# Kernel tuning notes

Hardware: AMD Instinct MI355X
Metric: run time of the kernel (lower is better)

Reference implementation:

```python
import jax, jax.numpy as jnp
import numpy as np

DECAY = 0.99
EPS = 1e-05


def setup_inputs() -> dict:
    key = jax.random.key(0)
    k1, k2 = jax.random.split(key)
    B, L, D, K = 8, 2048, 512, 4096
    x = jax.random.normal(k1, (B, L, D), dtype=jnp.float32)
    # variance_scaling(scale=1, fan_in, uniform): U(-limit, limit), limit = sqrt(3/fan_in)
    limit = np.sqrt(3.0 / D)
    codebook = jax.random.uniform(k2, (K, D), dtype=jnp.float32, minval=-limit, maxval=limit)
    return {
        "x": x,
        "codebook": codebook,
        "hidden_cluster": jnp.zeros((K,), jnp.float32),
        "hidden_dw": jnp.zeros((K, D), jnp.float32),
        "count": jnp.zeros((), jnp.float32),
    }


def reference(x, codebook, hidden_cluster, hidden_dw, count):
    K, D = codebook.shape
    B, L, _ = x.shape
    # avoids materializing the (B,L,K,D) broadcast the naive cdist creates)
    x2 = jnp.sum(x * x, axis=-1, keepdims=True)                  # (B,L,1)
    c2 = jnp.sum(codebook * codebook, axis=-1)                   # (K,)
    xc = jnp.einsum("bld,kd->blk", x, codebook)                  # (B,L,K)
    d2 = x2 - 2.0 * xc + c2
    indices = jnp.argmin(d2, axis=-1)                            # (B,L) int
    flat_idx = indices.reshape(-1)

    # cluster_counts = one_hot(indices).sum((0,1)) as a scatter-add
    cluster_counts = jnp.zeros((K,), jnp.float32).at[flat_idx].add(1.0)
    # dw = einsum('bln,bld->nd', one_hot, x) as a scatter-add of x rows
    dw = jnp.zeros((K, D), jnp.float32).at[flat_idx].add(x.reshape(-1, D))

    decay = jnp.asarray(DECAY, x.dtype)
    one = jnp.ones([], x.dtype)
    count_new = count + 1.0
    bias = one - decay ** count_new

    hidden_cluster_new = hidden_cluster * decay + (one - decay) * cluster_counts
    avg_cluster = hidden_cluster_new / bias
    hidden_dw_new = hidden_dw * decay + (one - decay) * dw
    avg_dw = hidden_dw_new / bias

    N = jnp.sum(avg_cluster)
    cc = (avg_cluster + EPS) / (N + K * EPS) * N
    codebook_new = avg_dw / cc[:, None]

    # quantized = one_hot(indices) @ codebook_new == gather
    q = codebook_new[indices]                                    # (B,L,D)
    quantized = x + jax.lax.stop_gradient(q - x)
    # optax.l2_loss(x, quantized).mean() == 0.5*(x-quantized)^2 mean
    codebook_loss = 0.5 * jnp.mean(jnp.square(x - quantized))
    return quantized, codebook_loss, indices
```

## Files before the change

### kernel.cpp

```cpp
#include <hip/hip_runtime.h>
#include <math.h>

#define BL 16384
#define D  512
#define K  4096
#define NCHB 8
#define XLOFF 8388608

#define OFF_C2    0
#define OFF_X2    (16<<10)
#define OFF_CNT   (80<<10)
#define OFF_AVGC  (96<<10)
#define OFF_SCAL  (112<<10)
#define OFF_IDX16 (116<<10)
#define OFF_KEYS  (160<<10)
#define OFF_CAND  (288<<10)
#define OFF_CBP   (576<<10)
#define OFF_CBN_FB (256<<10)

typedef _Float16 f16x8 __attribute__((ext_vector_type(8)));
typedef float    f32x4 __attribute__((ext_vector_type(4)));
#define MFMA16(a,b,c) __builtin_amdgcn_mfma_f32_16x16x32_f16(a,b,c,0,0,0)


__global__ void rowsq_all(const float* __restrict__ x, const float* __restrict__ cb,
                          float* __restrict__ x2, float* __restrict__ c2)
{
    int b    = blockIdx.x;
    int lane = threadIdx.x;
    const float* p; float* o; int row;
    if (b < K) { p = cb; o = c2; row = b; }
    else       { p = x;  o = x2; row = b - K; }
    p += (size_t)row * D;
    float s = 0.f;
#pragma unroll
    for (int j = 0; j < D / 64; ++j) {
        float v = p[lane + j * 64];
        s = fmaf(v, v, s);
    }
#pragma unroll
    for (int off = 32; off > 0; off >>= 1)
        s += __shfl_down(s, off, 64);
    if (lane == 0) o[row] = s;
}

__global__ __launch_bounds__(256) void rescore_kernel(
    const float* __restrict__ x, const float* __restrict__ cb,
    const float* __restrict__ x2, const float* __restrict__ c2,
    const unsigned short* __restrict__ cand,
    unsigned long long* __restrict__ keys,
    float* __restrict__ counts, unsigned short* __restrict__ idx16)
{
    int t = blockIdx.x * 256 + threadIdx.x;
    int row = t >> 3, ci = t & 7;
    int idx = cand[(size_t)row * 8 + ci];
    const float* xp = x  + (size_t)row * D;
    const float* cp = cb + (size_t)idx * D;
    float acc = 0.f;
#pragma unroll 4
    for (int k0 = 0; k0 < D; k0 += 4) {
        float4 xv = *(const float4*)(xp + k0);
        float4 cv = *(const float4*)(cp + k0);
        acc = fmaf(xv.x, cv.x, acc);
        acc = fmaf(xv.y, cv.y, acc);
        acc = fmaf(xv.z, cv.z, acc);
        acc = fmaf(xv.w, cv.w, acc);
    }
    float wv = x2[row] - 2.0f * acc;
    float dd = wv + c2[idx];
    unsigned long long key =
        ((unsigned long long)__float_as_uint(dd) << 12) | (unsigned long long)idx;
#pragma unroll
    for (int m = 1; m < 8; m <<= 1) {
        unsigned long long o = __shfl_xor(key, m, 64);
        key = o < key ? o : key;
    }
    if ((t & 7) == 0) {
        keys[row] = key;
        int kf = (int)(key & 0xFFFULL);
        idx16[row] = (unsigned short)kf;
        atomicAdd(&counts[kf], 1.0f);
    }
}


__device__ __forceinline__ void load_lds16(const unsigned short* g, unsigned short* l) {
    __builtin_amdgcn_global_load_lds(
        (const __attribute__((address_space(1))) unsigned int*)(g),
        (__attribute__((address_space(3))) unsigned int*)(l), 16, 0, 0);
}

__global__ __launch_bounds__(256) void split_interleave(
    const float* __restrict__ x, const float* __restrict__ cb,
    unsigned short* __restrict__ xp, unsigned short* __restrict__ cbp)
{
    int gw   = blockIdx.x * 4 + (threadIdx.x >> 6);
    int lane = threadIdx.x & 63;
    int rl   = lane >> 3;
    int p    = lane & 7;
    const float* src; int nr, c, r0; bool isX;
    if (gw < 16384) { c = gw >> 11; r0 = (gw & 2047) * 8; src = x;  nr = BL; isX = true; }
    else { int lw = gw - 16384; c = lw >> 9; r0 = (lw & 511) * 8; src = cb; nr = K; isX = false; }
    int r = r0 + rl;
    int g = p ^ rl;
    const float* sp = src + (size_t)r * D + c * 64 + g * 8;
    float4 f0 = *(const float4*)sp, f1 = *(const float4*)(sp + 4);
    float f[8] = {f0.x,f0.y,f0.z,f0.w,f1.x,f1.y,f1.z,f1.w};
    __align__(16) _Float16 oh[8], ol[8];
#pragma unroll
    for (int i = 0; i < 8; ++i) {
        _Float16 h = (_Float16)f[i];
        oh[i] = h;
        ol[i] = (_Float16)(f[i] - (float)h);
    }
    size_t off = ((size_t)(c * nr + r) * 8 + p) * 8;
    if (isX) {
        *(uint4*)(xp + off)         = *(const uint4*)oh;
        *(uint4*)(xp + XLOFF + off) = *(const uint4*)ol;
    } else {
        *(uint4*)(cbp + off) = *(const uint4*)oh;
    }
}

__global__ __launch_bounds__(256, 2) void argmin_mfma(
    const unsigned short* __restrict__ xp, const unsigned short* __restrict__ cbp,
    const float* __restrict__ x2, const float* __restrict__ c2,
    unsigned short* __restrict__ cand)
{
    __shared__ __align__(16) unsigned short sAh[128 * 64];
    __shared__ __align__(16) unsigned short sAl[128 * 64];
    __shared__ __align__(16) unsigned short sB [128 * 64];

    const int tid = threadIdx.x;
    const int l   = tid & 63;
    const int w   = tid >> 6;
    const int wm  = w >> 1, wn = w & 1;
    const int q   = l >> 4;
    const int cc  = l & 15;
    const int row0 = blockIdx.x * 128;
    const int nb   = blockIdx.y * 1024;

    int rdA[4], rdB[4];
#pragma unroll
    for (int t = 0; t < 4; ++t) {
        int ra = wm * 64 + t * 16 + cc;
        int rb = wn * 64 + t * 16 + cc;
        rdA[t] = ra * 128 + ((q ^ (ra & 7)) * 16);
        rdB[t] = rb * 128 + ((q ^ (rb & 7)) * 16);
    }

    unsigned long long k1[16], k2[16];
#pragma unroll
    for (int s = 0; s < 16; ++s) { k1[s] = ~0ULL; k2[s] = ~0ULL; }

    for (int n0 = 0; n0 < 8; ++n0) {
        f32x4 acc[4][4];
#pragma unroll
        for (int tm = 0; tm < 4; ++tm)
#pragma unroll
            for (int tn = 0; tn < 4; ++tn) { f32x4 z = {0.f,0.f,0.f,0.f}; acc[tm][tn] = z; }

        for (int c = 0; c < NCHB; ++c) {
            __syncthreads();
            {
                size_t abase = ((size_t)c * BL + row0) * 64;
                size_t bbase = ((size_t)c * K + nb + n0 * 128) * 64;
#pragma unroll
                for (int i = 0; i < 12; ++i) {
                    int gi = i * 4 + w;
                    if (gi < 16)
                        load_lds16(xp + abase + gi * 512 + l * 8, &sAh[gi * 512 + l * 8]);
                    else if (gi < 32) {
                        int ga = gi - 16;
                        load_lds16(xp + XLOFF + abase + ga * 512 + l * 8, &sAl[ga * 512 + l * 8]);
                    } else {
                        int gb = gi - 32;
                        load_lds16(cbp + bbase + gb * 512 + l * 8, &sB[gb * 512 + l * 8]);
                    }
                }
            }
            __syncthreads();
#pragma unroll
            for (int kh = 0; kh < 2; ++kh) {
                const int xo = kh * 64;
                f16x8 Ah[4], Al[4], Bf[4];
#pragma unroll
                for (int t = 0; t < 4; ++t) {
                    Ah[t] = *(const f16x8*)((const char*)sAh + (rdA[t] ^ xo));
                    Al[t] = *(const f16x8*)((const char*)sAl + (rdA[t] ^ xo));
                    Bf[t] = *(const f16x8*)((const char*)sB  + (rdB[t] ^ xo));
                }
#pragma unroll
                for (int tm = 0; tm < 4; ++tm)
#pragma unroll
                    for (int tn = 0; tn < 4; ++tn) {
                        acc[tm][tn] = MFMA16(Ah[tm], Bf[tn], acc[tm][tn]);
                        acc[tm][tn] = MFMA16(Al[tm], Bf[tn], acc[tm][tn]);
                    }
            }
        }
        float c2v[4];
#pragma unroll
        for (int tn = 0; tn < 4; ++tn)
            c2v[tn] = c2[nb + n0 * 128 + wn * 64 + tn * 16 + cc];
#pragma unroll
        for (int tm = 0; tm < 4; ++tm)
#pragma unroll
            for (int r = 0; r < 4; ++r) {
                int s = tm * 4 + r;
                float x2v = x2[row0 + wm * 64 + tm * 16 + q * 4 + r];
#pragma unroll
                for (int tn = 0; tn < 4; ++tn) {
                    unsigned col = nb + n0 * 128 + wn * 64 + tn * 16 + cc;
                    float dd = (x2v - 2.0f * acc[tm][tn][r]) + c2v[tn];
                    unsigned long long key =
                        ((unsigned long long)__float_as_uint(dd) << 12) | col;
                    if (key < k1[s]) { k2[s] = k1[s]; k1[s] = key; }
                    else if (key < k2[s]) { k2[s] = key; }
                }
            }
    }

#pragma unroll
    for (int s = 0; s < 16; ++s) {
#pragma unroll
        for (int m = 1; m < 16; m <<= 1) {
            unsigned long long o1 = __shfl_xor(k1[s], m, 64);
            unsigned long long o2 = __shfl_xor(k2[s], m, 64);
            unsigned long long lf = k1[s] > o1 ? k1[s] : o1;
            unsigned long long ws_ = k2[s] < o2 ? k2[s] : o2;
            k1[s] = k1[s] < o1 ? k1[s] : o1;
            k2[s] = lf < ws_ ? lf : ws_;
        }
    }

    __syncthreads();
    unsigned long long* sc = (unsigned long long*)sAh;
    if (cc == 0) {
#pragma unroll
        for (int s = 0; s < 16; ++s) {
            int rl = wm * 64 + (s >> 2) * 16 + q * 4 + (s & 3);
            sc[(rl * 2 + wn) * 2 + 0] = k1[s];
            sc[(rl * 2 + wn) * 2 + 1] = k2[s];
        }
    }
    __syncthreads();
    if (tid < 128) {
        unsigned long long pa1 = sc[(tid * 2 + 0) * 2 + 0], pa2 = sc[(tid * 2 + 0) * 2 + 1];
        unsigned long long pb1 = sc[(tid * 2 + 1) * 2 + 0], pb2 = sc[(tid * 2 + 1) * 2 + 1];
        unsigned long long m1 = pa1 < pb1 ? pa1 : pb1;
        unsigned long long lf = pa1 > pb1 ? pa1 : pb1;
        unsigned long long ws_ = pa2 < pb2 ? pa2 : pb2;
        unsigned long long m2 = lf < ws_ ? lf : ws_;
        size_t base = (size_t)(row0 + tid) * 8 + blockIdx.y * 2;
        cand[base + 0] = (unsigned short)(m1 & 0xFFFULL);
        cand[base + 1] = (unsigned short)(m2 & 0xFFFULL);
    }
}

__global__ __launch_bounds__(256) void argmin_fb(
    const float* __restrict__ x, const float* __restrict__ cb,
    const float* __restrict__ x2, const float* __restrict__ c2,
    unsigned long long* __restrict__ keys)
{
    __shared__ __align__(16) float As[32][68];
    __shared__ __align__(16) float Bs[32][68];
    __shared__ float rv[64][16];
    __shared__ int   ri[64][16];

    const int tid  = threadIdx.x;
    const int tx   = tid & 15;
    const int ty   = tid >> 4;
    const int row0 = blockIdx.x * 64;
    const int nb   = blockIdx.y * 1024;

    float x2r[4];
#pragma unroll
    for (int m = 0; m < 4; ++m) x2r[m] = x2[row0 + ty * 4 + m];

    float minv[4]; int mini[4];
#pragma unroll
    for (int m = 0; m < 4; ++m) { minv[m] = 3.4028235e38f; mini[m] = 0; }

    for (int n0 = 0; n0 < 1024; n0 += 64) {
        float acc[4][4];
#pragma unroll
        for (int m = 0; m < 4; ++m)
#pragma unroll
            for (int n = 0; n < 4; ++n) acc[m][n] = 0.f;

        for (int d0 = 0; d0 < D; d0 += 32) {
            __syncthreads();
#pragma unroll
            for (int j = 0; j < 2; ++j) {
                int v   = j * 256 + tid;
                int row = v >> 3;
                int col = (v & 7) * 4;
                float4 av = *(const float4*)(x  + (size_t)(row0 + row) * D + d0 + col);
                As[col + 0][row] = av.x; As[col + 1][row] = av.y;
                As[col + 2][row] = av.z; As[col + 3][row] = av.w;
                float4 bv = *(const float4*)(cb + (size_t)(nb + n0 + row) * D + d0 + col);
                Bs[col + 0][row] = bv.x; Bs[col + 1][row] = bv.y;
                Bs[col + 2][row] = bv.z; Bs[col + 3][row] = bv.w;
            }
            __syncthreads();
#pragma unroll
            for (int kk = 0; kk < 32; ++kk) {
                float4 a4 = *(const float4*)&As[kk][ty * 4];
                float4 b4 = *(const float4*)&Bs[kk][tx * 4];
                float a_[4] = { a4.x, a4.y, a4.z, a4.w };
                float b_[4] = { b4.x, b4.y, b4.z, b4.w };
#pragma unroll
                for (int m = 0; m < 4; ++m)
#pragma unroll
                    for (int n = 0; n < 4; ++n)
                        acc[m][n] = fmaf(a_[m], b_[n], acc[m][n]);
            }
        }
#pragma unroll
        for (int n = 0; n < 4; ++n) {
            int kidx = nb + n0 + tx * 4 + n;
            float c2k = c2[kidx];
#pragma unroll
            for (int m = 0; m < 4; ++m) {
                float wv = x2r[m] - 2.0f * acc[m][n];
                float dd = wv + c2k;
                if (dd < minv[m]) { minv[m] = dd; mini[m] = kidx; }
            }
        }
    }
#pragma unroll
    for (int m = 0; m < 4; ++m) { rv[ty * 4 + m][tx] = minv[m]; ri[ty * 4 + m][tx] = mini[m]; }
    __syncthreads();
    if (tid < 64) {
        float bv = rv[tid][0]; int bi = ri[tid][0];
#pragma unroll
        for (int j = 1; j < 16; ++j) {
            float v = rv[tid][j]; int ii = ri[tid][j];
            if (v < bv || (v == bv && ii < bi)) { bv = v; bi = ii; }
        }
        unsigned long long key =
            ((unsigned long long)__float_as_uint(bv) << 12) | (unsigned long long)bi;
        atomicMin(&keys[row0 + tid], key);
    }
}


__global__ void count_kernel(const unsigned long long* __restrict__ keys,
                             float* __restrict__ counts, unsigned short* __restrict__ idx16)
{
    int i = blockIdx.x * 256 + threadIdx.x;
    int k = (int)(keys[i] & 0xFFFULL);
    idx16[i] = (unsigned short)k;
    atomicAdd(&counts[k], 1.0f);
}

__global__ __launch_bounds__(256) void ema_cluster_kernel(
    const float* __restrict__ hc, const float* __restrict__ counts,
    const float* __restrict__ countp, float* __restrict__ avgc, float* __restrict__ Nout)
{
    __shared__ float sm[256];
    int i = blockIdx.x * 256 + threadIdx.x;
    const float om = 1.0f - 0.99f;
    float bias = 1.0f - powf(0.99f, countp[0] + 1.0f);
    float a = (hc[i] * 0.99f + om * counts[i]) / bias;
    avgc[i] = a;
    sm[threadIdx.x] = a;
    __syncthreads();
    for (int s = 128; s > 0; s >>= 1) {
        if (threadIdx.x < s) sm[threadIdx.x] += sm[threadIdx.x + s];
        __syncthreads();
    }
    if (threadIdx.x == 0) atomicAdd(Nout, sm[0]);
}

__global__ __launch_bounds__(256) void code_update_kernel(
    const float* __restrict__ x, const unsigned short* __restrict__ idx16,
    const float* __restrict__ hdw, const float* __restrict__ avgc,
    const float* __restrict__ Nptr, const float* __restrict__ countp,
    float* __restrict__ cbn)
{
    __shared__ unsigned short rows[2048];
    __shared__ int cnt;
    int k = blockIdx.x, tid = threadIdx.x;
    if (tid == 0) cnt = 0;
    __syncthreads();
    const uint4* ip = (const uint4*)idx16;
    for (int j = 0; j < 8; ++j) {
        int u = j * 256 + tid;
        uint4 v = ip[u];
        unsigned ww[4] = {v.x, v.y, v.z, v.w};
#pragma unroll
        for (int e = 0; e < 4; ++e) {
            int k0 = (int)(ww[e] & 0xFFFFu), k1 = (int)(ww[e] >> 16);
            if (k0 == k) { int p = atomicAdd(&cnt, 1); if (p < 2048) rows[p] = (unsigned short)(u * 8 + e * 2); }
            if (k1 == k) { int p = atomicAdd(&cnt, 1); if (p < 2048) rows[p] = (unsigned short)(u * 8 + e * 2 + 1); }
        }
    }
    __syncthreads();
    int n = cnt < 2048 ? cnt : 2048;
    float a0 = 0.f, a1 = 0.f;
    for (int p = 0; p < n; ++p) {
        int r = rows[p];
        a0 += x[(size_t)r * D + tid];
        a1 += x[(size_t)r * D + tid + 256];
    }
    const float om = 1.0f - 0.99f;
    float bias = 1.0f - powf(0.99f, countp[0] + 1.0f);
    float Nv = *Nptr;
    float ccv = ((avgc[k] + 1e-5f) / (Nv + 0.04096f)) * Nv;
    size_t b = (size_t)k * D;
    cbn[b + tid]       = ((hdw[b + tid]       * 0.99f + om * a0) / bias) / ccv;
    cbn[b + tid + 256] = ((hdw[b + tid + 256] * 0.99f + om * a1) / bias) / ccv;
}

__global__ __launch_bounds__(256) void gather_kernel(
    const float* __restrict__ x, const unsigned long long* __restrict__ keys,
    const float* __restrict__ cbn, float* __restrict__ outq,
    float* __restrict__ partial)
{
    __shared__ float sm[256];
    int row = blockIdx.x;
    int tid = threadIdx.x;
    int k   = (int)(keys[row] & 0xFFFULL);
    const float* xpp = x   + (size_t)row * D;
    const float* cp  = cbn + (size_t)k   * D;
    float* op = outq + (size_t)row * D;
    float local = 0.f;
#pragma unroll
    for (int j = 0; j < 2; ++j) {
        int d = tid + j * 256;
        float xv = xpp[d];
        float qv = cp[d];
        float quant = xv + (qv - xv);
        op[d] = quant;
        float diff = xv - quant;
        local = fmaf(diff, diff, local);
    }
    sm[tid] = local;
    __syncthreads();
    for (int s = 128; s > 0; s >>= 1) {
        if (tid < s) sm[tid] += sm[tid + s];
        __syncthreads();
    }
    if (tid == 0) {
        partial[row] = sm[0];
        outq[8388609 + row] = (float)k;
    }
}

__global__ __launch_bounds__(256) void finalize_kernel(
    const float* __restrict__ partial, float* __restrict__ out)
{
    __shared__ double sm[256];
    int tid = threadIdx.x;
    double s = 0.0;
#pragma unroll
    for (int j = 0; j < 64; ++j) s += (double)partial[tid + j * 256];
    sm[tid] = s;
    __syncthreads();
    for (int st = 128; st > 0; st >>= 1) {
        if (tid < st) sm[tid] += sm[tid + st];
        __syncthreads();
    }
    if (tid == 0) out[8388608] = (float)(0.5 * sm[0] / 8388608.0);
}


extern "C" void kernel_launch(void* const* d_in, const int* in_sizes, int n_in,
                              void* d_out, int out_size, void* d_ws, size_t ws_size,
                              hipStream_t stream)
{
    const float* x   = (const float*)d_in[0];
    const float* cb  = (const float*)d_in[1];
    const float* hc  = (const float*)d_in[2];
    const float* hdw = (const float*)d_in[3];
    const float* cnt = (const float*)d_in[4];
    float* out = (float*)d_out;

    char* ws = (char*)d_ws;
    float*  c2     = (float*)(ws + OFF_C2);
    float*  x2     = (float*)(ws + OFF_X2);
    float*  counts = (float*)(ws + OFF_CNT);
    float*  avgc   = (float*)(ws + OFF_AVGC);
    float*  Nout   = (float*)(ws + OFF_SCAL + 8);
    unsigned short* idx16 = (unsigned short*)(ws + OFF_IDX16);
    unsigned long long* keys = (unsigned long long*)(ws + OFF_KEYS);
    float*  partial= (float*)(ws + OFF_X2);

    hipMemsetAsync(ws + OFF_CNT, 0, (32 << 10) + 16, stream);

    rowsq_all<<<K + BL, 64, 0, stream>>>(x, cb, x2, c2);

    const bool primary = ws_size >= ((size_t)10 << 20);
    float* cbn;
    if (primary) {
        unsigned short* gxp = (unsigned short*)d_out;
        unsigned short* gcp = (unsigned short*)(ws + OFF_CBP);
        unsigned short* cand = (unsigned short*)(ws + OFF_CAND);
        cbn = (float*)(ws + OFF_CBP);

        split_interleave<<<5120, 256, 0, stream>>>(x, cb, gxp, gcp);
        argmin_mfma<<<dim3(BL / 128, 4), 256, 0, stream>>>(gxp, gcp, x2, c2, cand);
        rescore_kernel<<<(BL * 8) / 256, 256, 0, stream>>>(x, cb, x2, c2, cand, keys,
                                                           counts, idx16);
    } else {
        cbn = (float*)(ws + OFF_CBN_FB);
        hipMemsetAsync(ws + OFF_KEYS, 0xFF, BL * 8, stream);
        argmin_fb<<<dim3(BL / 64, 4), 256, 0, stream>>>(x, cb, x2, c2, keys);
        count_kernel<<<BL / 256, 256, 0, stream>>>(keys, counts, idx16);
    }

    ema_cluster_kernel<<<K / 256, 256, 0, stream>>>(hc, counts, cnt, avgc, Nout);
    code_update_kernel<<<K, 256, 0, stream>>>(x, idx16, hdw, avgc, Nout, cnt, cbn);
    gather_kernel<<<BL, 256, 0, stream>>>(x, keys, cbn, out, partial);
    finalize_kernel<<<1, 256, 0, stream>>>(partial, out);
}
```

Baseline: 332.8 us.

## Double-buffer argmin MFMA loads with 8-wave blocks and interleaved compute phases

Rewrites the argmin GEMM main loop to use 512-thread blocks (2x4 waves), a 256-column N tile and double-buffered LDS. Global-to-LDS copies for the next k-chunk are issued in four slices, each overlapping one MFMA phase, with explicit waitcnt, barriers and raised wave priority around the MFMAs. c2 and x2 are staged in LDS once per block, and the final reduction now merges four wave partials. The aim is to hide memory latency behind MFMA work and drop the two full block syncs per chunk. In exchange it uses more LDS (128 KB buffers) and more barriers, and the hand-written wait counts add a risk of ordering errors.

Measured after the change: 349.5 us. +5.0%, slower.

```diff
diff --git a/kernel.cpp b/kernel.cpp
--- a/kernel.cpp
+++ b/kernel.cpp
@@ -122,23 +122,30 @@
     }
 }
 
-__global__ __launch_bounds__(256, 2) void argmin_mfma(
+__global__ __launch_bounds__(512, 2) void argmin_mfma(
     const unsigned short* __restrict__ xp, const unsigned short* __restrict__ cbp,
     const float* __restrict__ x2, const float* __restrict__ c2,
     unsigned short* __restrict__ cand)
 {
-    __shared__ __align__(16) unsigned short sAh[128 * 64];
-    __shared__ __align__(16) unsigned short sAl[128 * 64];
-    __shared__ __align__(16) unsigned short sB [128 * 64];
+    __shared__ __align__(16) unsigned short buf[2 * 32768];
+    __shared__ __align__(16) float c2s[1024];
+    __shared__ __align__(16) float x2s[128];
+
+#define AH_OFF 0
+#define AL_OFF 16384
+#define B_OFF  32768
 
     const int tid = threadIdx.x;
     const int l   = tid & 63;
-    const int w   = tid >> 6;
-    const int wm  = w >> 1, wn = w & 1;
     const int q   = l >> 4;
     const int cc  = l & 15;
+    const int w   = tid >> 6;
+    const int wm  = w >> 2;
+    const int wn  = w & 3;
     const int row0 = blockIdx.x * 128;
     const int nb   = blockIdx.y * 1024;
+
+    char* sb = (char*)buf;
 
     int rdA[4], rdB[4];
 #pragma unroll
@@ -149,76 +156,173 @@
         rdB[t] = rb * 128 + ((q ^ (rb & 7)) * 16);
     }
 
+    if (tid < 128) x2s[tid] = x2[row0 + tid];
+#pragma unroll
+    for (int j = 0; j < 2; ++j) c2s[tid + j * 512] = c2[nb + tid + j * 512];
+    {
+        const unsigned short* sAh0 = xp + ((size_t)row0 << 6);
+        const unsigned short* sAl0 = sAh0 + XLOFF;
+        const unsigned short* sB0  = cbp + ((size_t)nb << 6);
+#pragma unroll
+        for (int i = 0; i < 2; ++i) {
+            load_lds16(sAh0 + i * 4096 + tid * 8,
+                       (unsigned short*)(sb + AH_OFF + i * 8192 + tid * 16));
+            load_lds16(sAl0 + i * 4096 + tid * 8,
+                       (unsigned short*)(sb + AL_OFF + i * 8192 + tid * 16));
+        }
+#pragma unroll
+        for (int i = 0; i < 4; ++i)
+            load_lds16(sB0 + i * 4096 + tid * 8,
+                       (unsigned short*)(sb + B_OFF + i * 8192 + tid * 16));
+    }
+    asm volatile("s_waitcnt vmcnt(0) lgkmcnt(0)" ::: "memory");
+    __builtin_amdgcn_s_barrier();
+
     unsigned long long k1[16], k2[16];
 #pragma unroll
     for (int s = 0; s < 16; ++s) { k1[s] = ~0ULL; k2[s] = ~0ULL; }
 
-    for (int n0 = 0; n0 < 8; ++n0) {
-        f32x4 acc[4][4];
+    f32x4 acc[4][4];
+#pragma unroll
+    for (int tm = 0; tm < 4; ++tm)
+#pragma unroll
+        for (int tn = 0; tn < 4; ++tn) { f32x4 z = {0.f,0.f,0.f,0.f}; acc[tm][tn] = z; }
+
+#pragma unroll 1
+    for (int it = 0; it < 32; ++it) {
+        const bool pf = (it < 31);
+        const int  br = (it & 1) << 16;
+        const int  bw = br ^ 65536;
+        const int  it1 = it + 1;
+        const int  c1  = it1 & 7;
+        const int  n01 = (it1 >> 3) & 3;
+        const unsigned short* srcAh = xp + ((size_t)(c1 * BL + row0) << 6);
+        const unsigned short* srcAl = srcAh + XLOFF;
+        const unsigned short* srcB  = cbp + ((size_t)(c1 * K + nb + n01 * 256) << 6);
+
+        f16x8 Ah[4], Bf[4];
+#pragma unroll
+        for (int t = 0; t < 4; ++t) {
+            Ah[t] = *(const f16x8*)(sb + br + AH_OFF + rdA[t]);
+            Bf[t] = *(const f16x8*)(sb + br + B_OFF  + rdB[t]);
+        }
+        if (pf) {
+#pragma unroll
+            for (int i = 0; i < 2; ++i)
+                load_lds16(srcAh + i * 4096 + tid * 8,
+                           (unsigned short*)(sb + bw + AH_OFF + i * 8192 + tid * 16));
+            asm volatile("s_waitcnt vmcnt(2)" ::: "memory");
+        } else {
+            asm volatile("s_waitcnt vmcnt(0)" ::: "memory");
+        }
+        __builtin_amdgcn_s_barrier();
+        asm volatile("s_waitcnt lgkmcnt(0)" ::: "memory");
+        __builtin_amdgcn_sched_barrier(0);
+        __builtin_amdgcn_s_setprio(1);
 #pragma unroll
         for (int tm = 0; tm < 4; ++tm)
 #pragma unroll
-            for (int tn = 0; tn < 4; ++tn) { f32x4 z = {0.f,0.f,0.f,0.f}; acc[tm][tn] = z; }
-
-        for (int c = 0; c < NCHB; ++c) {
-            __syncthreads();
-            {
-                size_t abase = ((size_t)c * BL + row0) * 64;
-                size_t bbase = ((size_t)c * K + nb + n0 * 128) * 64;
-#pragma unroll
-                for (int i = 0; i < 12; ++i) {
-                    int gi = i * 4 + w;
-                    if (gi < 16)
-                        load_lds16(xp + abase + gi * 512 + l * 8, &sAh[gi * 512 + l * 8]);
-                    else if (gi < 32) {
-                        int ga = gi - 16;
-                        load_lds16(xp + XLOFF + abase + ga * 512 + l * 8, &sAl[ga * 512 + l * 8]);
-                    } else {
-                        int gb = gi - 32;
-                        load_lds16(cbp + bbase + gb * 512 + l * 8, &sB[gb * 512 + l * 8]);
+            for (int tn = 0; tn < 4; ++tn)
+                acc[tm][tn] = MFMA16(Ah[tm], Bf[tn], acc[tm][tn]);
+        __builtin_amdgcn_s_setprio(0);
+        __builtin_amdgcn_s_barrier();
+
+        f16x8 Al[4];
+#pragma unroll
+        for (int t = 0; t < 4; ++t)
+            Al[t] = *(const f16x8*)(sb + br + AL_OFF + rdA[t]);
+        if (pf) {
+#pragma unroll
+            for (int i = 0; i < 2; ++i)
+                load_lds16(srcB + i * 4096 + tid * 8,
+                           (unsigned short*)(sb + bw + B_OFF + i * 8192 + tid * 16));
+        }
+        __builtin_amdgcn_s_barrier();
+        asm volatile("s_waitcnt lgkmcnt(0)" ::: "memory");
+        __builtin_amdgcn_sched_barrier(0);
+        __builtin_amdgcn_s_setprio(1);
+#pragma unroll
+        for (int tm = 0; tm < 4; ++tm)
+#pragma unroll
+            for (int tn = 0; tn < 4; ++tn)
+                acc[tm][tn] = MFMA16(Al[tm], Bf[tn], acc[tm][tn]);
+        __builtin_amdgcn_s_setprio(0);
+        __builtin_amdgcn_s_barrier();
+
+        f16x8 Ah1[4], Bg[4];
+#pragma unroll
+        for (int t = 0; t < 4; ++t) {
+            Ah1[t] = *(const f16x8*)(sb + br + AH_OFF + (rdA[t] ^ 64));
+            Bg[t]  = *(const f16x8*)(sb + br + B_OFF  + (rdB[t] ^ 64));
+        }
+        if (pf) {
+#pragma unroll
+            for (int i = 2; i < 4; ++i)
+                load_lds16(srcB + i * 4096 + tid * 8,
+                           (unsigned short*)(sb + bw + B_OFF + i * 8192 + tid * 16));
+        }
+        __builtin_amdgcn_s_barrier();
+        asm volatile("s_waitcnt lgkmcnt(0)" ::: "memory");
+        __builtin_amdgcn_sched_barrier(0);
+        __builtin_amdgcn_s_setprio(1);
+#pragma unroll
+        for (int tm = 0; tm < 4; ++tm)
+#pragma unroll
+            for (int tn = 0; tn < 4; ++tn)
+                acc[tm][tn] = MFMA16(Ah1[tm], Bg[tn], acc[tm][tn]);
+        __builtin_amdgcn_s_setprio(0);
+        __builtin_amdgcn_s_barrier();
+
+        f16x8 Al1[4];
+#pragma unroll
+        for (int t = 0; t < 4; ++t)
+            Al1[t] = *(const f16x8*)(sb + br + AL_OFF + (rdA[t] ^ 64));
+        if (pf) {
+#pragma unroll
+            for (int i = 0; i < 2; ++i)
+                load_lds16(srcAl + i * 4096 + tid * 8,
+                           (unsigned short*)(sb + bw + AL_OFF + i * 8192 + tid * 16));
+            asm volatile("s_waitcnt vmcnt(2)" ::: "memory");
+        }
+        __builtin_amdgcn_s_barrier();
+        asm volatile("s_waitcnt lgkmcnt(0)" ::: "memory");
+        __builtin_amdgcn_sched_barrier(0);
+        __builtin_amdgcn_s_setprio(1);
+#pragma unroll
+        for (int tm = 0; tm < 4; ++tm)
+#pragma unroll
+            for (int tn = 0; tn < 4; ++tn)
+                acc[tm][tn] = MFMA16(Al1[tm], Bg[tn], acc[tm][tn]);
+        __builtin_amdgcn_s_setprio(0);
+        __builtin_amdgcn_s_barrier();
+
+        if ((it & 7) == 7) {
+            const int n0 = it >> 3;
+            float c2v[4];
+#pragma unroll
+            for (int tn = 0; tn < 4; ++tn)
+                c2v[tn] = c2s[n0 * 256 + wn * 64 + tn * 16 + cc];
+#pragma unroll
+            for (int tm = 0; tm < 4; ++tm)
+#pragma unroll
+                for (int r = 0; r < 4; ++r) {
+                    const int s = tm * 4 + r;
+                    float x2v = x2s[wm * 64 + tm * 16 + q * 4 + r];
+#pragma unroll
+                    for (int tn = 0; tn < 4; ++tn) {
+                        unsigned col = nb + n0 * 256 + wn * 64 + tn * 16 + cc;
+                        float dd = (x2v - 2.0f * acc[tm][tn][r]) + c2v[tn];
+                        unsigned long long key =
+                            ((unsigned long long)__float_as_uint(dd) << 12) | col;
+                        if (key < k1[s]) { k2[s] = k1[s]; k1[s] = key; }
+                        else if (key < k2[s]) { k2[s] = key; }
                     }
                 }
-            }
-            __syncthreads();
-#pragma unroll
-            for (int kh = 0; kh < 2; ++kh) {
-                const int xo = kh * 64;
-                f16x8 Ah[4], Al[4], Bf[4];
-#pragma unroll
-                for (int t = 0; t < 4; ++t) {
-                    Ah[t] = *(const f16x8*)((const char*)sAh + (rdA[t] ^ xo));
-                    Al[t] = *(const f16x8*)((const char*)sAl + (rdA[t] ^ xo));
-                    Bf[t] = *(const f16x8*)((const char*)sB  + (rdB[t] ^ xo));
-                }
-#pragma unroll
-                for (int tm = 0; tm < 4; ++tm)
-#pragma unroll
-                    for (int tn = 0; tn < 4; ++tn) {
-                        acc[tm][tn] = MFMA16(Ah[tm], Bf[tn], acc[tm][tn]);
-                        acc[tm][tn] = MFMA16(Al[tm], Bf[tn], acc[tm][tn]);
-                    }
-            }
-        }
-        float c2v[4];
-#pragma unroll
-        for (int tn = 0; tn < 4; ++tn)
-            c2v[tn] = c2[nb + n0 * 128 + wn * 64 + tn * 16 + cc];
-#pragma unroll
-        for (int tm = 0; tm < 4; ++tm)
-#pragma unroll
-            for (int r = 0; r < 4; ++r) {
-                int s = tm * 4 + r;
-                float x2v = x2[row0 + wm * 64 + tm * 16 + q * 4 + r];
-#pragma unroll
-                for (int tn = 0; tn < 4; ++tn) {
-                    unsigned col = nb + n0 * 128 + wn * 64 + tn * 16 + cc;
-                    float dd = (x2v - 2.0f * acc[tm][tn][r]) + c2v[tn];
-                    unsigned long long key =
-                        ((unsigned long long)__float_as_uint(dd) << 12) | col;
-                    if (key < k1[s]) { k2[s] = k1[s]; k1[s] = key; }
-                    else if (key < k2[s]) { k2[s] = key; }
-                }
-            }
+#pragma unroll
+            for (int tm = 0; tm < 4; ++tm)
+#pragma unroll
+                for (int tn = 0; tn < 4; ++tn) { f32x4 z = {0.f,0.f,0.f,0.f}; acc[tm][tn] = z; }
+        }
     }
 
 #pragma unroll
@@ -235,23 +339,28 @@
     }
 
     __syncthreads();
-    unsigned long long* sc = (unsigned long long*)sAh;
+    unsigned long long* sc = (unsigned long long*)buf;
     if (cc == 0) {
 #pragma unroll
         for (int s = 0; s < 16; ++s) {
             int rl = wm * 64 + (s >> 2) * 16 + q * 4 + (s & 3);
-            sc[(rl * 2 + wn) * 2 + 0] = k1[s];
-            sc[(rl * 2 + wn) * 2 + 1] = k2[s];
+            sc[(rl * 4 + wn) * 2 + 0] = k1[s];
+            sc[(rl * 4 + wn) * 2 + 1] = k2[s];
         }
     }
     __syncthreads();
     if (tid < 128) {
-        unsigned long long pa1 = sc[(tid * 2 + 0) * 2 + 0], pa2 = sc[(tid * 2 + 0) * 2 + 1];
-        unsigned long long pb1 = sc[(tid * 2 + 1) * 2 + 0], pb2 = sc[(tid * 2 + 1) * 2 + 1];
-        unsigned long long m1 = pa1 < pb1 ? pa1 : pb1;
-        unsigned long long lf = pa1 > pb1 ? pa1 : pb1;
-        unsigned long long ws_ = pa2 < pb2 ? pa2 : pb2;
-        unsigned long long m2 = lf < ws_ ? lf : ws_;
+        unsigned long long m1 = sc[(tid * 4 + 0) * 2 + 0];
+        unsigned long long m2 = sc[(tid * 4 + 0) * 2 + 1];
+#pragma unroll
+        for (int j = 1; j < 4; ++j) {
+            unsigned long long b1 = sc[(tid * 4 + j) * 2 + 0];
+            unsigned long long b2 = sc[(tid * 4 + j) * 2 + 1];
+            unsigned long long lf = m1 > b1 ? m1 : b1;
+            unsigned long long ws_ = m2 < b2 ? m2 : b2;
+            m1 = m1 < b1 ? m1 : b1;
+            m2 = lf < ws_ ? lf : ws_;
+        }
         size_t base = (size_t)(row0 + tid) * 8 + blockIdx.y * 2;
         cand[base + 0] = (unsigned short)(m1 & 0xFFFULL);
         cand[base + 1] = (unsigned short)(m2 & 0xFFFULL);
@@ -501,7 +610,7 @@
         cbn = (float*)(ws + OFF_CBP);
 
         split_interleave<<<5120, 256, 0, stream>>>(x, cb, gxp, gcp);
-        argmin_mfma<<<dim3(BL / 128, 4), 256, 0, stream>>>(gxp, gcp, x2, c2, cand);
+        argmin_mfma<<<dim3(BL / 128, 4), 512, 0, stream>>>(gxp, gcp, x2, c2, cand);
         rescore_kernel<<<(BL * 8) / 256, 256, 0, stream>>>(x, cb, x2, c2, cand, keys,
                                                            counts, idx16);
     } else {
```

## Widen argmin MFMA tile to 128x256 per block with per-pass top-2 reduction

Applied to the files above, without the earlier changes.

The argmin kernel now covers 256 codebook columns per outer pass instead of 128. Each wave holds a 4x8 accumulator tile, which halves the number of A (x hi/lo) reloads from global memory to LDS. The top-2 reduction is moved inside each pass, keeping only four packed candidate pairs per lane rather than 16 per-row pairs, and x2/c2 are staged in LDS. The costs are higher accumulator register pressure and a larger LDS footprint, which may lower occupancy below the two blocks per CU requested by the launch bounds.

Result: faster. 323.8 us (-2.7%).

```diff
diff --git a/kernel.cpp b/kernel.cpp
--- a/kernel.cpp
+++ b/kernel.cpp
@@ -129,129 +129,160 @@
 {
     __shared__ __align__(16) unsigned short sAh[128 * 64];
     __shared__ __align__(16) unsigned short sAl[128 * 64];
-    __shared__ __align__(16) unsigned short sB [128 * 64];
+    __shared__ __align__(16) unsigned short sB [256 * 64];
+    __shared__ __align__(16) float c2s[1024];
+    __shared__ float x2s[128];
 
     const int tid = threadIdx.x;
     const int l   = tid & 63;
     const int w   = tid >> 6;
-    const int wm  = w >> 1, wn = w & 1;
+    const int wm  = w >> 1;
+    const int wn  = w & 1;
     const int q   = l >> 4;
     const int cc  = l & 15;
     const int row0 = blockIdx.x * 128;
     const int nb   = blockIdx.y * 1024;
 
-    int rdA[4], rdB[4];
+    if (tid < 128) x2s[tid] = x2[row0 + tid];
+#pragma unroll
+    for (int j = 0; j < 4; ++j) c2s[j * 256 + tid] = c2[nb + j * 256 + tid];
+
+    int rdA[4], rdB[8];
 #pragma unroll
     for (int t = 0; t < 4; ++t) {
         int ra = wm * 64 + t * 16 + cc;
-        int rb = wn * 64 + t * 16 + cc;
         rdA[t] = ra * 128 + ((q ^ (ra & 7)) * 16);
+    }
+#pragma unroll
+    for (int t = 0; t < 8; ++t) {
+        int rb = wn * 128 + t * 16 + cc;
         rdB[t] = rb * 128 + ((q ^ (rb & 7)) * 16);
     }
 
-    unsigned long long k1[16], k2[16];
-#pragma unroll
-    for (int s = 0; s < 16; ++s) { k1[s] = ~0ULL; k2[s] = ~0ULL; }
-
-    for (int n0 = 0; n0 < 8; ++n0) {
-        f32x4 acc[4][4];
+    unsigned long long s1a = ~0ULL, s2a = ~0ULL, s1b = ~0ULL, s2b = ~0ULL;
+    unsigned long long s1c = ~0ULL, s2c = ~0ULL, s1d = ~0ULL, s2d = ~0ULL;
+
+#pragma unroll 1
+    for (int n0 = 0; n0 < 4; ++n0) {
+        f32x4 acc[4][8];
 #pragma unroll
         for (int tm = 0; tm < 4; ++tm)
 #pragma unroll
-            for (int tn = 0; tn < 4; ++tn) { f32x4 z = {0.f,0.f,0.f,0.f}; acc[tm][tn] = z; }
-
+            for (int tn = 0; tn < 8; ++tn) { f32x4 z = {0.f,0.f,0.f,0.f}; acc[tm][tn] = z; }
+
+#pragma unroll 1
         for (int c = 0; c < NCHB; ++c) {
             __syncthreads();
             {
                 size_t abase = ((size_t)c * BL + row0) * 64;
-                size_t bbase = ((size_t)c * K + nb + n0 * 128) * 64;
-#pragma unroll
-                for (int i = 0; i < 12; ++i) {
-                    int gi = i * 4 + w;
-                    if (gi < 16)
-                        load_lds16(xp + abase + gi * 512 + l * 8, &sAh[gi * 512 + l * 8]);
-                    else if (gi < 32) {
-                        int ga = gi - 16;
-                        load_lds16(xp + XLOFF + abase + ga * 512 + l * 8, &sAl[ga * 512 + l * 8]);
-                    } else {
-                        int gb = gi - 32;
-                        load_lds16(cbp + bbase + gb * 512 + l * 8, &sB[gb * 512 + l * 8]);
-                    }
+                size_t bbase = ((size_t)(c * K + nb + n0 * 256)) * 64;
+#pragma unroll
+                for (int i = 0; i < 4; ++i) {
+                    load_lds16(xp + abase + i * 2048 + tid * 8, &sAh[i * 2048 + tid * 8]);
+                    load_lds16(xp + XLOFF + abase + i * 2048 + tid * 8, &sAl[i * 2048 + tid * 8]);
                 }
+#pragma unroll
+                for (int i = 0; i < 8; ++i)
+                    load_lds16(cbp + bbase + i * 2048 + tid * 8, &sB[i * 2048 + tid * 8]);
             }
             __syncthreads();
 #pragma unroll
             for (int kh = 0; kh < 2; ++kh) {
                 const int xo = kh * 64;
-                f16x8 Ah[4], Al[4], Bf[4];
+                f16x8 Ah[4], Al[4], Bf[8];
 #pragma unroll
                 for (int t = 0; t < 4; ++t) {
                     Ah[t] = *(const f16x8*)((const char*)sAh + (rdA[t] ^ xo));
                     Al[t] = *(const f16x8*)((const char*)sAl + (rdA[t] ^ xo));
-                    Bf[t] = *(const f16x8*)((const char*)sB  + (rdB[t] ^ xo));
                 }
 #pragma unroll
+                for (int t = 0; t < 8; ++t)
+                    Bf[t] = *(const f16x8*)((const char*)sB + (rdB[t] ^ xo));
+#pragma unroll
                 for (int tm = 0; tm < 4; ++tm)
 #pragma unroll
-                    for (int tn = 0; tn < 4; ++tn) {
+                    for (int tn = 0; tn < 8; ++tn)
                         acc[tm][tn] = MFMA16(Ah[tm], Bf[tn], acc[tm][tn]);
+#pragma unroll
+                for (int tm = 0; tm < 4; ++tm)
+#pragma unroll
+                    for (int tn = 0; tn < 8; ++tn)
                         acc[tm][tn] = MFMA16(Al[tm], Bf[tn], acc[tm][tn]);
+            }
+        }
+
+        {
+            unsigned long long k1[16], k2[16];
+#pragma unroll
+            for (int s = 0; s < 16; ++s) { k1[s] = ~0ULL; k2[s] = ~0ULL; }
+            float c2v[8];
+#pragma unroll
+            for (int tn = 0; tn < 8; ++tn)
+                c2v[tn] = c2s[n0 * 256 + wn * 128 + tn * 16 + cc];
+#pragma unroll
+            for (int tm = 0; tm < 4; ++tm)
+#pragma unroll
+                for (int r = 0; r < 4; ++r) {
+                    const int s = tm * 4 + r;
+                    float x2v = x2s[wm * 64 + tm * 16 + q * 4 + r];
+#pragma unroll
+                    for (int tn = 0; tn < 8; ++tn) {
+                        unsigned col = nb + n0 * 256 + wn * 128 + tn * 16 + cc;
+                        float dd = (x2v - 2.0f * acc[tm][tn][r]) + c2v[tn];
+                        unsigned long long key =
+                            ((unsigned long long)__float_as_uint(dd) << 12) | col;
+                        if (key < k1[s]) { k2[s] = k1[s]; k1[s] = key; }
+                        else if (key < k2[s]) { k2[s] = key; }
                     }
-            }
-        }
-        float c2v[4];
-#pragma unroll
-        for (int tn = 0; tn < 4; ++tn)
-            c2v[tn] = c2[nb + n0 * 128 + wn * 64 + tn * 16 + cc];
-#pragma unroll
-        for (int tm = 0; tm < 4; ++tm)
-#pragma unroll
-            for (int r = 0; r < 4; ++r) {
-                int s = tm * 4 + r;
-                float x2v = x2[row0 + wm * 64 + tm * 16 + q * 4 + r];
-#pragma unroll
-                for (int tn = 0; tn < 4; ++tn) {
-                    unsigned col = nb + n0 * 128 + wn * 64 + tn * 16 + cc;
-                    float dd = (x2v - 2.0f * acc[tm][tn][r]) + c2v[tn];
-                    unsigned long long key =
-                        ((unsigned long long)__float_as_uint(dd) << 12) | col;
-                    if (key < k1[s]) { k2[s] = k1[s]; k1[s] = key; }
-                    else if (key < k2[s]) { k2[s] = key; }
                 }
-            }
-    }
-
-#pragma unroll
-    for (int s = 0; s < 16; ++s) {
-#pragma unroll
-        for (int m = 1; m < 16; m <<= 1) {
-            unsigned long long o1 = __shfl_xor(k1[s], m, 64);
-            unsigned long long o2 = __shfl_xor(k2[s], m, 64);
-            unsigned long long lf = k1[s] > o1 ? k1[s] : o1;
-            unsigned long long ws_ = k2[s] < o2 ? k2[s] : o2;
-            k1[s] = k1[s] < o1 ? k1[s] : o1;
-            k2[s] = lf < ws_ ? lf : ws_;
+
+#pragma unroll
+            for (int s = 0; s < 16; ++s) {
+#pragma unroll
+                for (int m = 1; m < 16; m <<= 1) {
+                    unsigned long long o1 = __shfl_xor(k1[s], m, 64);
+                    unsigned long long o2 = __shfl_xor(k2[s], m, 64);
+                    unsigned long long lf = k1[s] > o1 ? k1[s] : o1;
+                    unsigned long long ws_ = k2[s] < o2 ? k2[s] : o2;
+                    k1[s] = k1[s] < o1 ? k1[s] : o1;
+                    k2[s] = lf < ws_ ? lf : ws_;
+                }
+            }
+            unsigned long long m1 = k1[0], m2 = k2[0];
+#pragma unroll
+            for (int s = 1; s < 16; ++s) {
+                if (cc == s) { m1 = k1[s]; m2 = k2[s]; }
+            }
+            if (n0 == 0)      { s1a = m1; s2a = m2; }
+            else if (n0 == 1) { s1b = m1; s2b = m2; }
+            else if (n0 == 2) { s1c = m1; s2c = m2; }
+            else              { s1d = m1; s2d = m2; }
         }
     }
 
     __syncthreads();
     unsigned long long* sc = (unsigned long long*)sAh;
-    if (cc == 0) {
-#pragma unroll
-        for (int s = 0; s < 16; ++s) {
-            int rl = wm * 64 + (s >> 2) * 16 + q * 4 + (s & 3);
-            sc[(rl * 2 + wn) * 2 + 0] = k1[s];
-            sc[(rl * 2 + wn) * 2 + 1] = k2[s];
-        }
+    {
+        int rloc = (cc >> 2) * 16 + q * 4 + (cc & 3);
+        int r    = wm * 64 + rloc;
+        size_t base = (size_t)((r * 2 + wn) * 4) * 2;
+        sc[base + 0] = s1a; sc[base + 1] = s2a;
+        sc[base + 2] = s1b; sc[base + 3] = s2b;
+        sc[base + 4] = s1c; sc[base + 5] = s2c;
+        sc[base + 6] = s1d; sc[base + 7] = s2d;
     }
     __syncthreads();
     if (tid < 128) {
-        unsigned long long pa1 = sc[(tid * 2 + 0) * 2 + 0], pa2 = sc[(tid * 2 + 0) * 2 + 1];
-        unsigned long long pb1 = sc[(tid * 2 + 1) * 2 + 0], pb2 = sc[(tid * 2 + 1) * 2 + 1];
-        unsigned long long m1 = pa1 < pb1 ? pa1 : pb1;
-        unsigned long long lf = pa1 > pb1 ? pa1 : pb1;
-        unsigned long long ws_ = pa2 < pb2 ? pa2 : pb2;
-        unsigned long long m2 = lf < ws_ ? lf : ws_;
+        unsigned long long m1 = ~0ULL, m2 = ~0ULL;
+#pragma unroll
+        for (int j = 0; j < 8; ++j) {
+            unsigned long long b1 = sc[(size_t)(tid * 8 + j) * 2 + 0];
+            unsigned long long b2 = sc[(size_t)(tid * 8 + j) * 2 + 1];
+            unsigned long long lf  = m1 > b1 ? m1 : b1;
+            unsigned long long ws_ = m2 < b2 ? m2 : b2;
+            m1 = m1 < b1 ? m1 : b1;
+            m2 = lf < ws_ ? lf : ws_;
+        }
         size_t base = (size_t)(row0 + tid) * 8 + blockIdx.y * 2;
         cand[base + 0] = (unsigned short)(m1 & 0xFFFULL);
         cand[base + 1] = (unsigned short)(m2 & 0xFFFULL);
```
